# Kernel tuning notes

Measured on AMD Instinct MI355X. Metric: run time of the kernel, lower is better.

The kernel has to match this reference:

```python
import jax, jax.numpy as jnp
import numpy as np

D = 64       # latent channels (d)
T = 512      # frame length, pinned by fc_1 = Linear(512*d//2, 512)
NUM_M = 64   # codebook size for source half (num_s = num_m)
NUM_N = 32   # codebook size for noise half (num_n = num_m // 2)
SCALE = 1.0  # soft-assignment temperature (self.scale)
K = 9        # BasicBlock conv kernel width


def conv1d(x, w, b):
    # x: (B, Cin, T), w: (Cout, Cin, K) -> (B, Cout, T), SAME padding
    y = jax.lax.conv_general_dilated(
        x, w, window_strides=(1,), padding='SAME',
        dimension_numbers=('NCH', 'OIH', 'NCH'))
    return y + b[None, :, None]


def basic_block(x, w1, b1, w2, b2, ws=None, bs=None):
    # Residual 1-D conv block: conv-relu-conv + shortcut, relu.
    h = jax.nn.relu(conv1d(x, w1, b1))
    h = conv1d(h, w2, b2)
    sc = x if ws is None else conv1d(x, ws, bs)
    return jax.nn.relu(h + sc)


def code_assign(x, means, scale):
    # VQ-style soft codebook assignment.
    # x: (B, C, T), means: (C, M)
    xt = jnp.swapaxes(x, 1, 2)  # (B, T, C)
    d2 = (jnp.sum(xt * xt, axis=-1, keepdims=True)
          - 2.0 * jnp.einsum('btc,cm->btm', xt, means)
          + jnp.sum(means * means, axis=0)[None, None, :])  # (B, T, M) squared dists
    prob = jax.nn.softmax(-scale * d2, axis=-1)              # soft assignment
    q = jnp.einsum('btm,cm->bct', prob, means)               # (B, C, T)
    arg_idx = jnp.argmin(d2, axis=-1)                        # (B, T) hard code index
    return q, arg_idx


def setup_inputs() -> dict:
    key = jax.random.key(0)
    ks = jax.random.split(key, 10)
    s = 0.05
    B = 1024
    return {
        'x': jax.random.normal(ks[0], (B, T), jnp.float32),
        'enc0_w1': jax.random.normal(ks[1], (D, 1, K), jnp.float32) * s,
        'enc0_b1': jnp.zeros((D,), jnp.float32),
        'enc0_w2': jax.random.normal(ks[2], (D, D, K), jnp.float32) * s,
        'enc0_b2': jnp.zeros((D,), jnp.float32),
        'enc0_ws': jax.random.normal(ks[3], (D, 1, 1), jnp.float32) * s,
        'enc0_bs': jnp.zeros((D,), jnp.float32),
        'enc_w': jax.random.normal(ks[4], (3, 2, D, D, K), jnp.float32) * s,
        'enc_b': jnp.zeros((3, 2, D), jnp.float32),
        'dec_w': jax.random.normal(ks[5], (3, 2, D // 2, D // 2, K), jnp.float32) * s,
        'dec_b': jnp.zeros((3, 2, D // 2), jnp.float32),
        'fc1_w': jax.random.normal(ks[6], (512, T * D // 2), jnp.float32) * 0.01,
        'fc1_b': jnp.zeros((512,), jnp.float32),
        'means_s': jax.random.uniform(ks[7], (D // 2, NUM_M), jnp.float32),
        'means_n': jax.random.uniform(ks[8], (D // 2, NUM_N), jnp.float32),
    }


def reference(x, enc0_w1, enc0_b1, enc0_w2, enc0_b2, enc0_ws, enc0_bs,
              enc_w, enc_b, dec_w, dec_b, fc1_w, fc1_b, means_s, means_n):
    # forward_half, stage == 1 (VQ coding active), soft=True
    B = x.shape[0]
    h = x[:, None, :]                                     # (B, 1, T)
    h = basic_block(h, enc0_w1, enc0_b1, enc0_w2, enc0_b2, enc0_ws, enc0_bs)
    h = jax.nn.relu(h)
    for i in range(3):
        h = basic_block(h, enc_w[i, 0], enc_b[i, 0], enc_w[i, 1], enc_b[i, 1])
    code_s = h[:, :D // 2, :]                             # (B, 32, T)
    code_n = h[:, D // 2:, :]
    q_s, idx_s = code_assign(code_s, means_s, SCALE)
    q_n, idx_n = code_assign(code_n, means_n, SCALE)

    def dec(z):
        for i in range(3):
            z = basic_block(z, dec_w[i, 0], dec_b[i, 0], dec_w[i, 1], dec_b[i, 1])
        flat = z.reshape(B, -1)                           # (B, T * D//2)
        return jnp.tanh(flat @ fc1_w.T + fc1_b)           # (B, 512)

    s_hat = dec(q_s)
    n_hat = dec(q_n)
    return s_hat, n_hat, idx_s, idx_n
```

## Files before the change

kernel.cpp:

```cpp
#include <hip/hip_runtime.h>
#include <math.h>


#define TB 512
#define BATCH 1024

__global__ __launch_bounds__(256) void transpose_w2_f64_kernel(
    const float* __restrict__ w, double* __restrict__ wT, int C, int nmat) {
  int total = nmat * C * C * 9;
  for (int i = blockIdx.x * blockDim.x + threadIdx.x; i < total;
       i += gridDim.x * blockDim.x) {
    int mat = i / (C * C * 9);
    int r = i % (C * C * 9);
    int cout = r / (C * 9);
    int rem = r % (C * 9);
    int cin = rem / 9;
    int k = rem % 9;
    wT[((mat * C + cin) * 9 + k) * C + cout] = (double)w[i];
  }
}

__global__ __launch_bounds__(256) void transpose_w_f32_kernel(
    const float* __restrict__ w, float* __restrict__ wT, int C, int nmat) {
  int total = nmat * C * C * 9;
  for (int i = blockIdx.x * blockDim.x + threadIdx.x; i < total;
       i += gridDim.x * blockDim.x) {
    int mat = i / (C * C * 9);
    int r = i % (C * C * 9);
    int cout = r / (C * 9);
    int rem = r % (C * 9);
    int cin = rem / 9;
    int k = rem % 9;
    wT[mat * C * C * 9 + (k * C + cin) * C + cout] = w[i];
  }
}

template <typename F>
__device__ __forceinline__ void conv64_fma_stream(const double* __restrict__ xr,
                                                  const double (&w)[9],
                                                  F&& upd) {
#pragma unroll
  for (int j2 = 0; j2 < 24; j2 += 2) {
    double2 v = *(const double2*)&xr[j2];
#pragma unroll
    for (int k = 0; k < 9; ++k) {
      int ta = j2 - k;
      if (ta >= 0 && ta < 16) upd(ta, w[k], v.x);
    }
#pragma unroll
    for (int k = 0; k < 9; ++k) {
      int tb = j2 + 1 - k;
      if (tb >= 0 && tb < 16) upd(tb, w[k], v.y);
    }
  }
}

__device__ __forceinline__ void load9(const double* __restrict__ p,
                                      double (&w)[9]) {
#pragma unroll
  for (int k = 0; k < 9; ++k) w[k] = p[k * 64];
}

__device__ __forceinline__ void conv64_body(const double* __restrict__ xs,
                                            const double* __restrict__ wT2,
                                            double acc[16], int lane,
                                            int wslab) {
  const double* wp0 = wT2 + lane;
  const double* xb = xs + wslab * 16;
  double wA[9], wB[9], wC[9], wD[9];
  load9(wp0, wA);
  load9(wp0 + 576, wB);
  auto upd = [&](int t, double w, double x) { acc[t] = fma(w, x, acc[t]); };
#pragma unroll 1
  for (int cin = 0; cin < 64; cin += 4) {
    load9(wp0 + (cin + 2) * 576, wC);
    load9(wp0 + (cin + 3) * 576, wD);
    conv64_fma_stream(xb + cin * 72, wA, upd);
    if (cin + 4 < 64) load9(wp0 + (cin + 4) * 576, wA);
    conv64_fma_stream(xb + (cin + 1) * 72, wB, upd);
    if (cin + 5 < 64) load9(wp0 + (cin + 5) * 576, wB);
    conv64_fma_stream(xb + (cin + 2) * 72, wC, upd);
    conv64_fma_stream(xb + (cin + 3) * 72, wD, upd);
  }
}

__global__ __launch_bounds__(256, 1) void enc0_f64_kernel(
    const float* __restrict__ x, const float* __restrict__ w1,
    const float* __restrict__ b1, const double* __restrict__ w2T,
    const float* __restrict__ b2, const float* __restrict__ wsc,
    const float* __restrict__ bsc, double* __restrict__ out) {
  __shared__ double xs0[80];
  __shared__ double w1s[576];
  __shared__ double b1s[64];
  __shared__ double mid[64 * 72];
  int b = blockIdx.y;
  int t0 = blockIdx.x * 64;
  int tid = threadIdx.x;
  if (tid < 80) {
    int t = t0 - 8 + tid;
    xs0[tid] = (t >= 0 && t < TB) ? (double)x[b * TB + t] : 0.0;
  }
  for (int i = tid; i < 576; i += 256) w1s[i] = (double)w1[i];
  if (tid < 64) b1s[tid] = (double)b1[tid];
  __syncthreads();
  for (int e = tid; e < 64 * 72; e += 256) {
    int cout = e / 72, tt = e % 72;
    int t = t0 - 4 + tt;
    double acc = b1s[cout];
#pragma unroll
    for (int k = 0; k < 9; ++k) acc = fma(w1s[cout * 9 + k], xs0[tt + k], acc);
    mid[e] = (t >= 0 && t < TB) ? fmax(acc, 0.0) : 0.0;
  }
  __syncthreads();
  int wave = tid >> 6;
  int lane = tid & 63;
  double acc[16];
  double bz = (double)b2[lane];
#pragma unroll
  for (int t = 0; t < 16; ++t) acc[t] = bz;
  conv64_body(mid, w2T, acc, lane, wave);
  __syncthreads();
  double* T = mid;
#pragma unroll
  for (int t = 0; t < 16; ++t) T[lane * 65 + wave * 16 + t] = acc[t];
  __syncthreads();
  for (int i = tid; i < 4096; i += 256) {
    int cout = i >> 6, tt = i & 63;
    double v = T[cout * 65 + tt] +
               fma((double)wsc[cout], xs0[8 + tt], (double)bsc[cout]);
    out[(b * 64 + cout) * TB + t0 + tt] = fmax(v, 0.0);
  }
}

template <bool SKIP>
__global__ __launch_bounds__(256, 1) void conv64_f64_kernel(
    const double* __restrict__ in, const double* __restrict__ wT2,
    const float* __restrict__ bias, const double* __restrict__ skip,
    double* __restrict__ out) {
  __shared__ double xs[64 * 72];
  int b = blockIdx.y;
  int t0 = blockIdx.x * 64;
  int tid = threadIdx.x;
  for (int i = tid; i < 64 * 72; i += 256) {
    int cin = i / 72, tt = i % 72;
    int t = t0 - 4 + tt;
    xs[i] = (t >= 0 && t < TB) ? in[(b * 64 + cin) * TB + t] : 0.0;
  }
  __syncthreads();
  int wave = tid >> 6;
  int lane = tid & 63;
  double acc[16];
  double bz = (double)bias[lane];
#pragma unroll
  for (int t = 0; t < 16; ++t) acc[t] = bz;
  conv64_body(xs, wT2, acc, lane, wave);
  __syncthreads();
  double* T = xs;
#pragma unroll
  for (int t = 0; t < 16; ++t) T[lane * 65 + wave * 16 + t] = acc[t];
  __syncthreads();
  for (int i = tid; i < 4096; i += 256) {
    int cout = i >> 6, tt = i & 63;
    double v = T[cout * 65 + tt];
    if constexpr (SKIP) v += skip[(b * 64 + cout) * TB + t0 + tt];
    out[(b * 64 + cout) * TB + t0 + tt] = fmax(v, 0.0);
  }
}

template <bool SKIP>
__global__ __launch_bounds__(256) void conv32z_kernel(
    const float* __restrict__ in0, const float* __restrict__ in1,
    const float* __restrict__ wT, const float* __restrict__ bias,
    const float* __restrict__ sk0, const float* __restrict__ sk1,
    float* __restrict__ o0, float* __restrict__ o1) {
  constexpr int XW = 136;
  __shared__ float xs[32 * XW];
  const float* in = blockIdx.z ? in1 : in0;
  const float* skip = blockIdx.z ? sk1 : sk0;
  float* out = blockIdx.z ? o1 : o0;
  int b = blockIdx.y;
  int t0 = blockIdx.x * 128;
  int tid = threadIdx.x;
  for (int i = tid; i < 32 * XW; i += 256) {
    int cin = i / XW, tt = i % XW;
    int t = t0 - 4 + tt;
    xs[i] = (t >= 0 && t < TB) ? in[(b * 32 + cin) * TB + t] : 0.f;
  }
  __syncthreads();
  int wave = __builtin_amdgcn_readfirstlane(tid >> 6);
  int lane = tid & 63;
  int cbase = (wave & 1) * 16;
  int ttl = (wave >> 1) * 64 + lane;
  float acc[16];
#pragma unroll
  for (int j = 0; j < 16; ++j) acc[j] = bias[cbase + j];
  for (int cin = 0; cin < 32; ++cin) {
#pragma unroll
    for (int k = 0; k < 9; ++k) {
      float xv = xs[cin * XW + ttl + k];
      const float* wp = wT + (k * 32 + cin) * 32 + cbase;
#pragma unroll
      for (int j = 0; j < 16; ++j) acc[j] = fmaf(xv, wp[j], acc[j]);
    }
  }
  int t = t0 + ttl;
#pragma unroll
  for (int j = 0; j < 16; ++j) {
    float v = acc[j];
    if constexpr (SKIP) v += skip[(b * 32 + cbase + j) * TB + t];
    out[(b * 32 + cbase + j) * TB + t] = fmaxf(v, 0.f);
  }
}

template <int M>
__global__ __launch_bounds__(256) void code_assign_kernel(
    const double* __restrict__ h, int coff, const float* __restrict__ means,
    float* __restrict__ q, float* __restrict__ idx_out) {
  __shared__ double ms[32 * M];
  __shared__ float msf[32 * M];
  __shared__ double msq[M];
  int b = blockIdx.y;
  int tid = threadIdx.x;
  int t = blockIdx.x * 256 + tid;
  for (int i = tid; i < 32 * M; i += 256) {
    float v = means[i];
    ms[i] = (double)v;
    msf[i] = v;
  }
  __syncthreads();
  if (tid < M) {
    double s = 0.0;
#pragma unroll
    for (int c = 0; c < 32; ++c) s = fma(ms[c * M + tid], ms[c * M + tid], s);
    msq[tid] = s;
  }
  __syncthreads();
  double xv[32];
  double sx = 0.0;
#pragma unroll
  for (int c = 0; c < 32; ++c) {
    xv[c] = h[(b * 64 + coff + c) * TB + t];
    sx = fma(xv[c], xv[c], sx);
  }
  double dmin = 1e300;
  int imin = 0;
  float ssum = 0.f;
  float qv[32];
#pragma unroll
  for (int c = 0; c < 32; ++c) qv[c] = 0.f;
  for (int m = 0; m < M; ++m) {
    double dot = 0.0;
#pragma unroll
    for (int c = 0; c < 32; ++c) dot = fma(xv[c], ms[c * M + m], dot);
    double d = sx - 2.0 * dot + msq[m];
    float p;
    if (d < dmin) {
      float f = expf((float)(d - dmin));
      ssum *= f;
#pragma unroll
      for (int c = 0; c < 32; ++c) qv[c] *= f;
      dmin = d;
      imin = m;
      p = 1.f;
    } else {
      p = expf((float)(dmin - d));
    }
    ssum += p;
#pragma unroll
    for (int c = 0; c < 32; ++c) qv[c] = fmaf(p, msf[c * M + m], qv[c]);
  }
  float inv = 1.f / ssum;
#pragma unroll
  for (int c = 0; c < 32; ++c) q[(b * 32 + c) * TB + t] = qv[c] * inv;
  idx_out[b * TB + t] = (float)imin;
}

__global__ __launch_bounds__(256) void fc_partial_gemm(
    const float* __restrict__ Z, const float* __restrict__ w,
    float* __restrict__ PB, int Mrows) {
  constexpr int BK = 32;
  constexpr int KC = 2048;
  __shared__ float As[BK][68];
  __shared__ float Bs[BK][68];
  int m0 = blockIdx.y * 64;
  int n0 = blockIdx.x * 64;
  int kbase = blockIdx.z * KC;
  int tid = threadIdx.x;
  int row = tid >> 2;
  int kq = (tid & 3) * 4;
  const float* zrow = Z + (size_t)(m0 + row) * 16384 + kbase;
  const float* wrow = w + (size_t)(n0 + row) * 16384 + kbase;
  int mg = tid >> 4;
  int ng = tid & 15;
  float acc[4][4] = {};
  for (int k0 = 0; k0 < KC; k0 += BK) {
    float4 a0 = *(const float4*)&zrow[k0 + kq];
    float4 a1 = *(const float4*)&zrow[k0 + kq + 16];
    float4 b0 = *(const float4*)&wrow[k0 + kq];
    float4 b1 = *(const float4*)&wrow[k0 + kq + 16];
    __syncthreads();
    As[kq + 0][row] = a0.x; As[kq + 1][row] = a0.y;
    As[kq + 2][row] = a0.z; As[kq + 3][row] = a0.w;
    As[kq + 16][row] = a1.x; As[kq + 17][row] = a1.y;
    As[kq + 18][row] = a1.z; As[kq + 19][row] = a1.w;
    Bs[kq + 0][row] = b0.x; Bs[kq + 1][row] = b0.y;
    Bs[kq + 2][row] = b0.z; Bs[kq + 3][row] = b0.w;
    Bs[kq + 16][row] = b1.x; Bs[kq + 17][row] = b1.y;
    Bs[kq + 18][row] = b1.z; Bs[kq + 19][row] = b1.w;
    __syncthreads();
#pragma unroll
    for (int kk = 0; kk < BK; ++kk) {
      float4 av = *(const float4*)&As[kk][mg * 4];
      float4 bv = *(const float4*)&Bs[kk][ng * 4];
      acc[0][0] = fmaf(av.x, bv.x, acc[0][0]);
      acc[0][1] = fmaf(av.x, bv.y, acc[0][1]);
      acc[0][2] = fmaf(av.x, bv.z, acc[0][2]);
      acc[0][3] = fmaf(av.x, bv.w, acc[0][3]);
      acc[1][0] = fmaf(av.y, bv.x, acc[1][0]);
      acc[1][1] = fmaf(av.y, bv.y, acc[1][1]);
      acc[1][2] = fmaf(av.y, bv.z, acc[1][2]);
      acc[1][3] = fmaf(av.y, bv.w, acc[1][3]);
      acc[2][0] = fmaf(av.z, bv.x, acc[2][0]);
      acc[2][1] = fmaf(av.z, bv.y, acc[2][1]);
      acc[2][2] = fmaf(av.z, bv.z, acc[2][2]);
      acc[2][3] = fmaf(av.z, bv.w, acc[2][3]);
      acc[3][0] = fmaf(av.w, bv.x, acc[3][0]);
      acc[3][1] = fmaf(av.w, bv.y, acc[3][1]);
      acc[3][2] = fmaf(av.w, bv.z, acc[3][2]);
      acc[3][3] = fmaf(av.w, bv.w, acc[3][3]);
    }
  }
  float* pbase = PB + (size_t)blockIdx.z * Mrows * 512;
#pragma unroll
  for (int mi = 0; mi < 4; ++mi) {
    float4 v = {acc[mi][0], acc[mi][1], acc[mi][2], acc[mi][3]};
    *(float4*)&pbase[(size_t)(m0 + mg * 4 + mi) * 512 + n0 + ng * 4] = v;
  }
}

__global__ __launch_bounds__(256) void fc_reduce_tanh(
    const float* __restrict__ PB, const float* __restrict__ bias,
    float* __restrict__ out, int Mrows, int rps, int c0) {
  constexpr int KS = 8;
  int idx = blockIdx.x * 256 + threadIdx.x;
  int m = idx >> 9, n = idx & 511;
  if (m >= Mrows) return;
  float s = bias[n];
#pragma unroll
  for (int ks = 0; ks < KS; ++ks)
    s += PB[((size_t)ks * Mrows + m) * 512 + n];
  int st = m / rps, rr = m - st * rps;
  out[((size_t)st * 1024 + c0 + rr) * 512 + n] = tanhf(s);
}

extern "C" void kernel_launch(void* const* d_in, const int* in_sizes, int n_in,
                              void* d_out, int out_size, void* d_ws,
                              size_t ws_size, hipStream_t stream) {
  const float* x = (const float*)d_in[0];
  const float* enc0_w1 = (const float*)d_in[1];
  const float* enc0_b1 = (const float*)d_in[2];
  const float* enc0_w2 = (const float*)d_in[3];
  const float* enc0_b2 = (const float*)d_in[4];
  const float* enc0_ws = (const float*)d_in[5];
  const float* enc0_bs = (const float*)d_in[6];
  const float* enc_w = (const float*)d_in[7];
  const float* enc_b = (const float*)d_in[8];
  const float* dec_w = (const float*)d_in[9];
  const float* dec_b = (const float*)d_in[10];
  const float* fc1_w = (const float*)d_in[11];
  const float* fc1_b = (const float*)d_in[12];
  const float* means_s = (const float*)d_in[13];
  const float* means_n = (const float*)d_in[14];

  const size_t WB = 2285568;
  int BC = 32;
  for (int c = 512; c >= 32; c >>= 1)
    if (WB + (size_t)c * 524288 <= ws_size) { BC = c; break; }

  double* wT0d = (double*)d_ws;
  double* wTed = wT0d + 36864;
  float* wTdf = (float*)(wTed + 221184);
  double* E0d = (double*)(wTdf + 55296);
  double* E1d = E0d + (size_t)BC * 32768;
  float* qs = (float*)E1d;
  float* qn = qs + (size_t)BC * 16384;
  float* D0s = qn + (size_t)BC * 16384;
  float* D0n = D0s + (size_t)BC * 16384;
  float* Dz = (float*)E0d;
  float* T1s = Dz + (size_t)2 * BC * 16384;
  float* T1n = T1s + (size_t)BC * 16384;
  float* PB = T1s;
  float* out = (float*)d_out;

  transpose_w2_f64_kernel<<<dim3(144), 256, 0, stream>>>(enc0_w2, wT0d, 64, 1);
  transpose_w2_f64_kernel<<<dim3(864), 256, 0, stream>>>(enc_w, wTed, 64, 6);
  transpose_w_f32_kernel<<<dim3(216), 256, 0, stream>>>(dec_w, wTdf, 32, 6);

  for (int c0 = 0; c0 < BATCH; c0 += BC) {
    const float* xb = x + (size_t)c0 * TB;

    enc0_f64_kernel<<<dim3(8, BC), 256, 0, stream>>>(
        xb, enc0_w1, enc0_b1, wT0d, enc0_b2, enc0_ws, enc0_bs, E0d);
    for (int i = 0; i < 3; ++i) {
      conv64_f64_kernel<false><<<dim3(8, BC), 256, 0, stream>>>(
          E0d, wTed + (2 * i) * 36864, enc_b + (2 * i) * 64, nullptr, E1d);
      conv64_f64_kernel<true><<<dim3(8, BC), 256, 0, stream>>>(
          E1d, wTed + (2 * i + 1) * 36864, enc_b + (2 * i + 1) * 64, E0d, E0d);
    }

    code_assign_kernel<64><<<dim3(2, BC), 256, 0, stream>>>(
        E0d, 0, means_s, qs, out + 2 * 524288 + (size_t)c0 * TB);
    code_assign_kernel<32><<<dim3(2, BC), 256, 0, stream>>>(
        E0d, 32, means_n, qn, out + 3 * 524288 + (size_t)c0 * TB);

    float* destS = Dz;
    float* destN = Dz + (size_t)BC * 16384;
    conv32z_kernel<false><<<dim3(4, BC, 2), 256, 0, stream>>>(
        qs, qn, wTdf + 0 * 9216, dec_b + 0 * 32, nullptr, nullptr, D0s, D0n);
    conv32z_kernel<true><<<dim3(4, BC, 2), 256, 0, stream>>>(
        D0s, D0n, wTdf + 1 * 9216, dec_b + 1 * 32, qs, qn, T1s, T1n);
    conv32z_kernel<false><<<dim3(4, BC, 2), 256, 0, stream>>>(
        T1s, T1n, wTdf + 2 * 9216, dec_b + 2 * 32, nullptr, nullptr, D0s, D0n);
    conv32z_kernel<true><<<dim3(4, BC, 2), 256, 0, stream>>>(
        D0s, D0n, wTdf + 3 * 9216, dec_b + 3 * 32, T1s, T1n, qs, qn);
    conv32z_kernel<false><<<dim3(4, BC, 2), 256, 0, stream>>>(
        qs, qn, wTdf + 4 * 9216, dec_b + 4 * 32, nullptr, nullptr, D0s, D0n);
    conv32z_kernel<true><<<dim3(4, BC, 2), 256, 0, stream>>>(
        D0s, D0n, wTdf + 5 * 9216, dec_b + 5 * 32, qs, qn, destS, destN);

    fc_partial_gemm<<<dim3(8, (2 * BC) / 64, 8), 256, 0, stream>>>(
        Dz, fc1_w, PB, 2 * BC);
    fc_reduce_tanh<<<dim3((2 * BC * 512) / 256), 256, 0, stream>>>(
        PB, fc1_b, out, 2 * BC, BC, c0);
  }
}
```

Measured before the change: 8.299 ms.

## Split encoder conv input channels across two wave groups with shared-memory reduction

The encoder f64 conv kernel now launches 512 threads instead of 256. Each of the four time slabs is handled by two waves, and each wave accumulates half of the 64 input channels. The partial sums are combined through shared memory before the transposed write-out. The weight prefetch pipeline is cut from four buffers to two to reduce register pressure. The aim is more waves per CU to hide FP64 FMA and weight-load latency, at the cost of extra syncs and LDS traffic for the reduction.

```diff
diff --git a/kernel.cpp b/kernel.cpp
--- a/kernel.cpp
+++ b/kernel.cpp
@@ -61,26 +61,20 @@
   for (int k = 0; k < 9; ++k) w[k] = p[k * 64];
 }
 
-__device__ __forceinline__ void conv64_body(const double* __restrict__ xs,
-                                            const double* __restrict__ wT2,
-                                            double acc[16], int lane,
-                                            int wslab) {
+__device__ __forceinline__ void conv64_body_range(
+    const double* __restrict__ xs, const double* __restrict__ wT2,
+    double acc[16], int lane, int wslab, int cin0) {
   const double* wp0 = wT2 + lane;
   const double* xb = xs + wslab * 16;
-  double wA[9], wB[9], wC[9], wD[9];
-  load9(wp0, wA);
-  load9(wp0 + 576, wB);
+  double wA[9], wB[9];
+  load9(wp0 + cin0 * 576, wA);
   auto upd = [&](int t, double w, double x) { acc[t] = fma(w, x, acc[t]); };
 #pragma unroll 1
-  for (int cin = 0; cin < 64; cin += 4) {
-    load9(wp0 + (cin + 2) * 576, wC);
-    load9(wp0 + (cin + 3) * 576, wD);
+  for (int cin = cin0; cin < cin0 + 32; cin += 2) {
+    load9(wp0 + (cin + 1) * 576, wB);
     conv64_fma_stream(xb + cin * 72, wA, upd);
-    if (cin + 4 < 64) load9(wp0 + (cin + 4) * 576, wA);
+    if (cin + 2 < cin0 + 32) load9(wp0 + (cin + 2) * 576, wA);
     conv64_fma_stream(xb + (cin + 1) * 72, wB, upd);
-    if (cin + 5 < 64) load9(wp0 + (cin + 5) * 576, wB);
-    conv64_fma_stream(xb + (cin + 2) * 72, wC, upd);
-    conv64_fma_stream(xb + (cin + 3) * 72, wD, upd);
   }
 }
 
@@ -118,7 +112,8 @@
   double bz = (double)b2[lane];
 #pragma unroll
   for (int t = 0; t < 16; ++t) acc[t] = bz;
-  conv64_body(mid, w2T, acc, lane, wave);
+  conv64_body_range(mid, w2T, acc, lane, wave, 0);
+  conv64_body_range(mid, w2T, acc, lane, wave, 32);
   __syncthreads();
   double* T = mid;
 #pragma unroll
@@ -133,35 +128,50 @@
 }
 
 template <bool SKIP>
-__global__ __launch_bounds__(256, 1) void conv64_f64_kernel(
+__global__ __launch_bounds__(512, 1) void conv64_f64_kernel(
     const double* __restrict__ in, const double* __restrict__ wT2,
     const float* __restrict__ bias, const double* __restrict__ skip,
     double* __restrict__ out) {
-  __shared__ double xs[64 * 72];
+  __shared__ double smem[64 * 72];
   int b = blockIdx.y;
   int t0 = blockIdx.x * 64;
   int tid = threadIdx.x;
-  for (int i = tid; i < 64 * 72; i += 256) {
+  for (int i = tid; i < 64 * 72; i += 512) {
     int cin = i / 72, tt = i % 72;
     int t = t0 - 4 + tt;
-    xs[i] = (t >= 0 && t < TB) ? in[(b * 64 + cin) * TB + t] : 0.0;
+    smem[i] = (t >= 0 && t < TB) ? in[(b * 64 + cin) * TB + t] : 0.0;
   }
   __syncthreads();
   int wave = tid >> 6;
   int lane = tid & 63;
+  int slab = wave & 3;
+  int half = wave >> 2;
   double acc[16];
-  double bz = (double)bias[lane];
-#pragma unroll
-  for (int t = 0; t < 16; ++t) acc[t] = bz;
-  conv64_body(xs, wT2, acc, lane, wave);
-  __syncthreads();
-  double* T = xs;
-#pragma unroll
-  for (int t = 0; t < 16; ++t) T[lane * 65 + wave * 16 + t] = acc[t];
-  __syncthreads();
-  for (int i = tid; i < 4096; i += 256) {
+  double init = half ? 0.0 : (double)bias[lane];
+#pragma unroll
+  for (int t = 0; t < 16; ++t) acc[t] = init;
+  conv64_body_range(smem, wT2, acc, lane, slab, half * 32);
+  __syncthreads();
+  if (half) {
+#pragma unroll
+    for (int t = 0; t < 16; ++t) smem[slab * 1024 + t * 64 + lane] = acc[t];
+  }
+  __syncthreads();
+  double fin[16];
+  if (!half) {
+#pragma unroll
+    for (int t = 0; t < 16; ++t)
+      fin[t] = acc[t] + smem[slab * 1024 + t * 64 + lane];
+  }
+  __syncthreads();
+  if (!half) {
+#pragma unroll
+    for (int t = 0; t < 16; ++t) smem[lane * 65 + slab * 16 + t] = fin[t];
+  }
+  __syncthreads();
+  for (int i = tid; i < 4096; i += 512) {
     int cout = i >> 6, tt = i & 63;
-    double v = T[cout * 65 + tt];
+    double v = smem[cout * 65 + tt];
     if constexpr (SKIP) v += skip[(b * 64 + cout) * TB + t0 + tt];
     out[(b * 64 + cout) * TB + t0 + tt] = fmax(v, 0.0);
   }
@@ -402,9 +412,9 @@
     enc0_f64_kernel<<<dim3(8, BC), 256, 0, stream>>>(
         xb, enc0_w1, enc0_b1, wT0d, enc0_b2, enc0_ws, enc0_bs, E0d);
     for (int i = 0; i < 3; ++i) {
-      conv64_f64_kernel<false><<<dim3(8, BC), 256, 0, stream>>>(
+      conv64_f64_kernel<false><<<dim3(8, BC), 512, 0, stream>>>(
           E0d, wTed + (2 * i) * 36864, enc_b + (2 * i) * 64, nullptr, E1d);
-      conv64_f64_kernel<true><<<dim3(8, BC), 256, 0, stream>>>(
+      conv64_f64_kernel<true><<<dim3(8, BC), 512, 0, stream>>>(
           E1d, wTed + (2 * i + 1) * 36864, enc_b + (2 * i + 1) * 64, E0d, E0d);
     }
 
```

After: 8.722 ms. 1.05x slower.
